# Performance work log

Hardware: AMD Instinct MI355X
Metric: run time of the kernel (lower is better)

## Reference

```python
import jax, jax.numpy as jnp
import numpy as np

N = 4_194_304
DT = 1800.0   # dt_s (30-minute steps)
G = 0.76      # solar transmittance g
AZ = 41.3     # glazed area Az


def setup_inputs() -> dict:
    key = jax.random.key(0)
    ks = jax.random.split(key, 16)
    f32 = jnp.float32
    def pos(k, lo, hi):  # positive scalar param
        return jax.random.uniform(k, (), dtype=f32, minval=lo, maxval=hi)
    return {
        # RC parameters (physically positive)
        "R_ie": pos(ks[0], 0.5, 2.0),
        "R_ea": pos(ks[1], 0.5, 2.0),
        "C_in": pos(ks[2], 1e6, 5e6),
        "C_en": pos(ks[3], 1e7, 5e7),
        "a_sol_in": pos(ks[4], 0.1, 0.9),
        "a_sol_en": pos(ks[5], 0.1, 0.9),
        "a_int_in": pos(ks[6], 0.1, 0.9),
        "a_int_en": pos(ks[7], 0.1, 0.9),
        "Tin0": jax.random.uniform(ks[8], (), dtype=f32, minval=18.0, maxval=22.0),
        # driver time series
        "To": jax.random.normal(ks[9], (N,), dtype=f32) * 5.0 + 10.0,
        "Irr": jax.random.uniform(ks[10], (N,), dtype=f32, maxval=800.0),
        "Qint": jax.random.uniform(ks[11], (N,), dtype=f32, maxval=500.0),
        "Qah": jax.random.uniform(ks[12], (N,), dtype=f32, maxval=3000.0),
        "Ria": jax.random.uniform(ks[13], (N,), dtype=f32, minval=0.05, maxval=0.5),
    }


def _simulate(R_ie, R_ea, C_in, C_en, a_sol_in, a_sol_en, a_int_in, a_int_en,
              Tin0, To, Irr, Qint, Qah, Ria):
    dt = jnp.float32(DT)
    Ria_c = jnp.maximum(Ria, 1e-6)                      # (n,)
    # A matrix entries (A22 varies per step via Ria)
    A11 = -(1.0 / R_ea + 1.0 / R_ie) / C_en             # scalar
    A12 = (1.0 / R_ie) / C_en                           # scalar
    A21 = (1.0 / R_ie) / C_in                           # scalar
    A22 = -(1.0 / Ria_c + 1.0 / R_ie) / C_in            # (n,)
    # M = I - dt*A, closed-form 2x2 inverse via determinant
    M11 = 1.0 - dt * A11                                # scalar
    M12 = -dt * A12                                     # scalar
    M21 = -dt * A21                                     # scalar
    M22 = 1.0 - dt * A22                                # (n,)
    det = M11 * M22 - M12 * M21                         # (n,)
    # dt * B @ u, vectorized over all steps
    Qsol = (G * AZ) * Irr                               # (n,)
    bu0 = dt * (To / (C_en * R_ea) + (a_sol_en / C_en) * Qsol + (a_int_en / C_en) * Qint)
    bu1 = dt * (To / (C_in * Ria_c) + (a_sol_in / C_in) * Qsol + (a_int_in / C_in) * Qint + Qah / C_in)

    def step(x, inp):
        b0, b1, m22, d = inp
        r0 = x[0] + b0
        r1 = x[1] + b1
        xn0 = (m22 * r0 - M12 * r1) / d
        xn1 = (-M21 * r0 + M11 * r1) / d
        return jnp.stack([xn0, xn1]), xn1

    x0 = jnp.stack([Tin0, Tin0])
    _, Tin_seq = jax.lax.scan(step, x0, (bu0, bu1, M22, det))
    return Tin_seq                                      # (n,) indoor temps


def reference(R_ie, R_ea, C_in, C_en, a_sol_in, a_sol_en, a_int_in, a_int_en,
              Tin0, To, Irr, Qint, Qah, Ria):
    return _simulate(R_ie, R_ea, C_in, C_en, a_sol_in, a_sol_en, a_int_in, a_int_en,
                     Tin0, To, Irr, Qint, Qah, Ria)
```

## Files before the change

kernel.cpp:

```cpp
#include <hip/hip_runtime.h>

#define BLOCK 256
#define SPAN_LB 4096
#define KITER 4
#define SPAN_FB 4096

struct Xf { float p, q, r, s, u, v; };

__device__ __forceinline__ Xf xf_id() {
    Xf t; t.p = 1.f; t.q = 0.f; t.r = 0.f; t.s = 1.f; t.u = 0.f; t.v = 0.f;
    return t;
}

__device__ __forceinline__ Xf xf_compose(const Xf& E, const Xf& L) {
    Xf o;
    o.p = L.p * E.p + L.q * E.r;
    o.q = L.p * E.q + L.q * E.s;
    o.r = L.r * E.p + L.s * E.r;
    o.s = L.r * E.q + L.s * E.s;
    o.u = L.p * E.u + L.q * E.v + L.u;
    o.v = L.r * E.u + L.s * E.v + L.v;
    return o;
}

struct Par {
    float M11, M12, M21, Kx;
    float c0, c1;
    float cTo0, cIrr0, cQi0;
    float cIrr1, cQi1;
};

__device__ __forceinline__ Par make_par(
    const float* pRie, const float* pRea, const float* pCin, const float* pCen,
    const float* pAsi, const float* pAse, const float* pAii, const float* pAie)
{
    const float dt = 1800.0f;
    const float GA = 0.76f * 41.3f;
    float R_ie = *pRie, R_ea = *pRea, C_in = *pCin, C_en = *pCen;
    float asi = *pAsi, ase = *pAse, aii = *pAii, aie = *pAie;
    Par P;
    float iRie = 1.0f / R_ie;
    P.M11 = 1.0f + dt * (1.0f / R_ea + iRie) / C_en;
    P.M12 = -(dt * iRie) / C_en;
    P.M21 = -(dt * iRie) / C_in;
    P.Kx  = P.M12 * P.M21;
    P.c1  = dt / C_in;
    P.c0  = 1.0f + P.c1 * iRie;
    P.cTo0  = dt / (C_en * R_ea);
    P.cIrr0 = dt * ase * GA / C_en;
    P.cQi0  = dt * aie / C_en;
    P.cIrr1 = dt * asi * GA / C_in;
    P.cQi1  = dt * aii / C_in;
    return P;
}

__device__ __forceinline__ void storeA(float* A, int s, const Xf& v) {
    float* b = A + 6 * s + (s >> 2);
    b[0] = v.p; b[1] = v.q; b[2] = v.r; b[3] = v.s; b[4] = v.u; b[5] = v.v;
}
__device__ __forceinline__ Xf loadA(const float* A, int s) {
    const float* b = A + 6 * s + (s >> 2);
    Xf v; v.p = b[0]; v.q = b[1]; v.r = b[2]; v.s = b[3]; v.u = b[4]; v.v = b[5];
    return v;
}
__device__ __forceinline__ void sm_store(float* sm, int i, const Xf& v) {
    float* b = sm + i * 7;
    b[0] = v.p; b[1] = v.q; b[2] = v.r; b[3] = v.s; b[4] = v.u; b[5] = v.v;
}
__device__ __forceinline__ Xf sm_load(const float* sm, int i) {
    const float* b = sm + i * 7;
    Xf v; v.p = b[0]; v.q = b[1]; v.r = b[2]; v.s = b[3]; v.u = b[4]; v.v = b[5];
    return v;
}

__device__ __forceinline__ Xf block_scan(Xf v, float* sm) {
    const int t = threadIdx.x;
    sm_store(sm, t, v);
    __syncthreads();
    for (int off = 1; off < BLOCK; off <<= 1) {
        Xf e;
        bool has = (t >= off);
        if (has) e = sm_load(sm, t - off);
        __syncthreads();
        if (has) { v = xf_compose(e, v); sm_store(sm, t, v); }
        __syncthreads();
    }
    return v;
}

__global__ __launch_bounds__(BLOCK, 4) void k_scan(
    const float* __restrict__ To, const float* __restrict__ Irr,
    const float* __restrict__ Qi, const float* __restrict__ Qa,
    const float* __restrict__ Ra,
    const float* pRie, const float* pRea, const float* pCin, const float* pCen,
    const float* pAsi, const float* pAse, const float* pAii, const float* pAie,
    const float* pTin0,
    unsigned int* __restrict__ flags, float* __restrict__ aggs,
    float* __restrict__ out, int N)
{
    __shared__ float smA[6400];
    __shared__ float smScan[BLOCK * 7];
    __shared__ float smE[6];
    const int t = threadIdx.x;
    const int b = blockIdx.x;
    const int blockBase = b * SPAN_LB;
    Par P = make_par(pRie, pRea, pCin, pCen, pAsi, pAse, pAii, pAie);

    float rRv[KITER][4], b0v[KITER][4], b1v[KITER][4];

#pragma unroll
    for (int k = 0; k < KITER; ++k) {
        const int s = t + BLOCK * k;
        const int gstep = blockBase + s * 4;
        float tox[4], irx[4], qix[4], qax[4], rax[4];
        if (gstep + 4 <= N) {
            float4 v;
            v = *(const float4*)(To  + gstep); tox[0]=v.x; tox[1]=v.y; tox[2]=v.z; tox[3]=v.w;
            v = *(const float4*)(Irr + gstep); irx[0]=v.x; irx[1]=v.y; irx[2]=v.z; irx[3]=v.w;
            v = *(const float4*)(Qi  + gstep); qix[0]=v.x; qix[1]=v.y; qix[2]=v.z; qix[3]=v.w;
            v = *(const float4*)(Qa  + gstep); qax[0]=v.x; qax[1]=v.y; qax[2]=v.z; qax[3]=v.w;
            v = *(const float4*)(Ra  + gstep); rax[0]=v.x; rax[1]=v.y; rax[2]=v.z; rax[3]=v.w;
        } else {
#pragma unroll
            for (int j = 0; j < 4; ++j) {
                int gi = gstep + j; bool val = gi < N;
                tox[j] = val ? To[gi]  : 0.f;
                irx[j] = val ? Irr[gi] : 0.f;
                qix[j] = val ? Qi[gi]  : 0.f;
                qax[j] = val ? Qa[gi]  : 0.f;
                rax[j] = val ? Ra[gi]  : 1.f;
            }
        }
        Xf sub = xf_id();
#pragma unroll
        for (int j = 0; j < 4; ++j) {
            float rR = __builtin_amdgcn_rcpf(fmaxf(rax[j], 1e-6f));
            float b0 = P.cTo0 * tox[j] + P.cIrr0 * irx[j] + P.cQi0 * qix[j];
            float b1 = P.c1 * fmaf(tox[j], rR, qax[j]) + P.cIrr1 * irx[j] + P.cQi1 * qix[j];
            rRv[k][j] = rR; b0v[k][j] = b0; b1v[k][j] = b1;
            if (gstep + j < N) {
                float M22 = fmaf(P.c1, rR, P.c0);
                float det = fmaf(P.M11, M22, -P.Kx);
                float rd  = __builtin_amdgcn_rcpf(det);
                Xf T;
                T.p =  M22 * rd;
                T.q = -P.M12 * rd;
                T.r = -P.M21 * rd;
                T.s =  P.M11 * rd;
                T.u = T.p * b0 + T.q * b1;
                T.v = T.r * b0 + T.s * b1;
                sub = xf_compose(sub, T);
            }
        }
        storeA(smA, s, sub);
    }
    __syncthreads();

    Xf w = xf_id();
#pragma unroll
    for (int j = 0; j < KITER; ++j) w = xf_compose(w, loadA(smA, KITER * t + j));
    Xf incl = block_scan(w, smScan);
    Xf E = (t > 0) ? sm_load(smScan, t - 1) : xf_id();

    if (t == BLOCK - 1) {
        float* dst = aggs + 6 * b;
        __hip_atomic_store(dst + 0, incl.p, __ATOMIC_RELAXED, __HIP_MEMORY_SCOPE_AGENT);
        __hip_atomic_store(dst + 1, incl.q, __ATOMIC_RELAXED, __HIP_MEMORY_SCOPE_AGENT);
        __hip_atomic_store(dst + 2, incl.r, __ATOMIC_RELAXED, __HIP_MEMORY_SCOPE_AGENT);
        __hip_atomic_store(dst + 3, incl.s, __ATOMIC_RELAXED, __HIP_MEMORY_SCOPE_AGENT);
        __hip_atomic_store(dst + 4, incl.u, __ATOMIC_RELAXED, __HIP_MEMORY_SCOPE_AGENT);
        __hip_atomic_store(dst + 5, incl.v, __ATOMIC_RELAXED, __HIP_MEMORY_SCOPE_AGENT);
        __hip_atomic_store(&flags[b], 1u, __ATOMIC_RELEASE, __HIP_MEMORY_SCOPE_AGENT);
    }

    if (b == 0) {
        if (t == 0) {
            smE[0] = 1.f; smE[1] = 0.f; smE[2] = 0.f;
            smE[3] = 1.f; smE[4] = 0.f; smE[5] = 0.f;
        }
    } else if (t < 64) {
        Xf acc = xf_id();
        for (int base = 0; base < b; base += 64) {
            const int idx = base + t;
            const bool has = (idx < b);
            for (;;) {
                bool ready = !has ||
                    (__hip_atomic_load(&flags[idx], __ATOMIC_ACQUIRE, __HIP_MEMORY_SCOPE_AGENT) != 0u);
                if (__all(ready)) break;
                __builtin_amdgcn_s_sleep(1);
            }
            Xf v = xf_id();
            if (has) {
                const float* src = aggs + 6 * idx;
                v.p = __hip_atomic_load(src + 0, __ATOMIC_RELAXED, __HIP_MEMORY_SCOPE_AGENT);
                v.q = __hip_atomic_load(src + 1, __ATOMIC_RELAXED, __HIP_MEMORY_SCOPE_AGENT);
                v.r = __hip_atomic_load(src + 2, __ATOMIC_RELAXED, __HIP_MEMORY_SCOPE_AGENT);
                v.s = __hip_atomic_load(src + 3, __ATOMIC_RELAXED, __HIP_MEMORY_SCOPE_AGENT);
                v.u = __hip_atomic_load(src + 4, __ATOMIC_RELAXED, __HIP_MEMORY_SCOPE_AGENT);
                v.v = __hip_atomic_load(src + 5, __ATOMIC_RELAXED, __HIP_MEMORY_SCOPE_AGENT);
            }
#pragma unroll
            for (int sft = 1; sft < 64; sft <<= 1) {
                Xf u;
                u.p = __shfl_up(v.p, sft, 64);
                u.q = __shfl_up(v.q, sft, 64);
                u.r = __shfl_up(v.r, sft, 64);
                u.s = __shfl_up(v.s, sft, 64);
                u.u = __shfl_up(v.u, sft, 64);
                u.v = __shfl_up(v.v, sft, 64);
                if (t >= sft) v = xf_compose(u, v);
            }
            Xf wacc;
            wacc.p = __shfl(v.p, 63, 64);
            wacc.q = __shfl(v.q, 63, 64);
            wacc.r = __shfl(v.r, 63, 64);
            wacc.s = __shfl(v.s, 63, 64);
            wacc.u = __shfl(v.u, 63, 64);
            wacc.v = __shfl(v.v, 63, 64);
            acc = xf_compose(acc, wacc);
        }
        if (t == 0) {
            smE[0] = acc.p; smE[1] = acc.q; smE[2] = acc.r;
            smE[3] = acc.s; smE[4] = acc.u; smE[5] = acc.v;
        }
    }
    __syncthreads();

    float T0 = *pTin0;
    float xb0 = (smE[0] + smE[1]) * T0 + smE[4];
    float xb1 = (smE[2] + smE[3]) * T0 + smE[5];

    float sx0 = E.p * xb0 + E.q * xb1 + E.u;
    float sx1 = E.r * xb0 + E.s * xb1 + E.v;
    float st0[KITER], st1[KITER];
#pragma unroll
    for (int j = 0; j < KITER; ++j) {
        st0[j] = sx0; st1[j] = sx1;
        Xf S = loadA(smA, KITER * t + j);
        float n0 = S.p * sx0 + S.q * sx1 + S.u;
        float n1 = S.r * sx0 + S.s * sx1 + S.v;
        sx0 = n0; sx1 = n1;
    }
    __syncthreads();
#pragma unroll
    for (int j = 0; j < KITER; ++j) {
        int s = KITER * t + j;
        float* pS = smA + 2 * s + (s >> 3);
        pS[0] = st0[j]; pS[1] = st1[j];
    }
    __syncthreads();

#pragma unroll
    for (int k = 0; k < KITER; ++k) {
        const int s = t + BLOCK * k;
        const float* pS = smA + 2 * s + (s >> 3);
        float x0 = pS[0], x1 = pS[1];
        const int gstep = blockBase + s * 4;
        float ov[4];
#pragma unroll
        for (int j = 0; j < 4; ++j) {
            float rR  = rRv[k][j];
            float M22 = fmaf(P.c1, rR, P.c0);
            float det = fmaf(P.M11, M22, -P.Kx);
            float rd  = __builtin_amdgcn_rcpf(det);
            float r0 = x0 + b0v[k][j];
            float r1 = x1 + b1v[k][j];
            float n0 = (M22 * r0 - P.M12 * r1) * rd;
            float n1 = (P.M11 * r1 - P.M21 * r0) * rd;
            x0 = n0; x1 = n1; ov[j] = n1;
        }
        if (gstep + 4 <= N) {
            float4 o; o.x = ov[0]; o.y = ov[1]; o.z = ov[2]; o.w = ov[3];
            *(float4*)(out + gstep) = o;
        } else {
#pragma unroll
            for (int j = 0; j < 4; ++j) { int gi = gstep + j; if (gi < N) out[gi] = ov[j]; }
        }
    }
}

__global__ __launch_bounds__(BLOCK, 4) void k_blocksum(
    const float* __restrict__ To, const float* __restrict__ Irr,
    const float* __restrict__ Qi, const float* __restrict__ Qa,
    const float* __restrict__ Ra,
    const float* pRie, const float* pRea, const float* pCin, const float* pCen,
    const float* pAsi, const float* pAse, const float* pAii, const float* pAie,
    Xf* __restrict__ blkX, int N)
{
    __shared__ float smA[6400];
    __shared__ float smScan[BLOCK * 7];
    const int t = threadIdx.x;
    const int blockBase = blockIdx.x * SPAN_FB;
    Par P = make_par(pRie, pRea, pCin, pCen, pAsi, pAse, pAii, pAie);

#pragma unroll
    for (int k = 0; k < 4; ++k) {
        const int s = t + BLOCK * k;
        const int gstep = blockBase + s * 4;
        float tox[4], irx[4], qix[4], qax[4], rax[4];
        if (gstep + 4 <= N) {
            float4 v;
            v = *(const float4*)(To  + gstep); tox[0]=v.x; tox[1]=v.y; tox[2]=v.z; tox[3]=v.w;
            v = *(const float4*)(Irr + gstep); irx[0]=v.x; irx[1]=v.y; irx[2]=v.z; irx[3]=v.w;
            v = *(const float4*)(Qi  + gstep); qix[0]=v.x; qix[1]=v.y; qix[2]=v.z; qix[3]=v.w;
            v = *(const float4*)(Qa  + gstep); qax[0]=v.x; qax[1]=v.y; qax[2]=v.z; qax[3]=v.w;
            v = *(const float4*)(Ra  + gstep); rax[0]=v.x; rax[1]=v.y; rax[2]=v.z; rax[3]=v.w;
        } else {
#pragma unroll
            for (int j = 0; j < 4; ++j) {
                int gi = gstep + j; bool val = gi < N;
                tox[j] = val ? To[gi]  : 0.f;
                irx[j] = val ? Irr[gi] : 0.f;
                qix[j] = val ? Qi[gi]  : 0.f;
                qax[j] = val ? Qa[gi]  : 0.f;
                rax[j] = val ? Ra[gi]  : 1.f;
            }
        }
        Xf sub = xf_id();
#pragma unroll
        for (int j = 0; j < 4; ++j) {
            if (gstep + j < N) {
                float rR  = __builtin_amdgcn_rcpf(fmaxf(rax[j], 1e-6f));
                float b0  = P.cTo0 * tox[j] + P.cIrr0 * irx[j] + P.cQi0 * qix[j];
                float b1  = P.c1 * fmaf(tox[j], rR, qax[j]) + P.cIrr1 * irx[j] + P.cQi1 * qix[j];
                float M22 = fmaf(P.c1, rR, P.c0);
                float det = fmaf(P.M11, M22, -P.Kx);
                float rd  = __builtin_amdgcn_rcpf(det);
                Xf T;
                T.p =  M22 * rd;
                T.q = -P.M12 * rd;
                T.r = -P.M21 * rd;
                T.s =  P.M11 * rd;
                T.u = T.p * b0 + T.q * b1;
                T.v = T.r * b0 + T.s * b1;
                sub = xf_compose(sub, T);
            }
        }
        storeA(smA, s, sub);
    }
    __syncthreads();

    Xf w = xf_id();
#pragma unroll
    for (int j = 0; j < 4; ++j) w = xf_compose(w, loadA(smA, 4 * t + j));
    Xf incl = block_scan(w, smScan);
    if (t == BLOCK - 1) blkX[blockIdx.x] = incl;
}

__global__ __launch_bounds__(BLOCK) void k_mid(
    const Xf* __restrict__ blkX, float2* __restrict__ blkSt,
    const float* pTin0, int NB)
{
    const int t = threadIdx.x;
    const int ser = (NB + BLOCK - 1) / BLOCK;
    const int base = t * ser;
    Xf acc = xf_id();
    for (int j = 0; j < ser; ++j) {
        int i = base + j;
        if (i < NB) acc = xf_compose(acc, blkX[i]);
    }
    __shared__ float sm[BLOCK * 7];
    block_scan(acc, sm);
    Xf E = xf_id();
    if (t > 0) E = sm_load(sm, t - 1);
    float T0 = *pTin0;
    float x0 = (E.p + E.q) * T0 + E.u;
    float x1 = (E.r + E.s) * T0 + E.v;
    for (int j = 0; j < ser; ++j) {
        int i = base + j;
        if (i < NB) {
            blkSt[i] = make_float2(x0, x1);
            Xf T = blkX[i];
            float n0 = T.p * x0 + T.q * x1 + T.u;
            float n1 = T.r * x0 + T.s * x1 + T.v;
            x0 = n0; x1 = n1;
        }
    }
}

__global__ __launch_bounds__(BLOCK, 4) void k_emit(
    const float* __restrict__ To, const float* __restrict__ Irr,
    const float* __restrict__ Qi, const float* __restrict__ Qa,
    const float* __restrict__ Ra,
    const float* pRie, const float* pRea, const float* pCin, const float* pCen,
    const float* pAsi, const float* pAse, const float* pAii, const float* pAie,
    const float2* __restrict__ blkSt, float* __restrict__ out, int N)
{
    __shared__ float smA[6400];
    __shared__ float smScan[BLOCK * 7];
    const int t = threadIdx.x;
    const int b = blockIdx.x;
    const int blockBase = b * SPAN_FB;
    Par P = make_par(pRie, pRea, pCin, pCen, pAsi, pAse, pAii, pAie);

    float rRv[4][4], b0v[4][4], b1v[4][4];

#pragma unroll
    for (int k = 0; k < 4; ++k) {
        const int s = t + BLOCK * k;
        const int gstep = blockBase + s * 4;
        float tox[4], irx[4], qix[4], qax[4], rax[4];
        if (gstep + 4 <= N) {
            float4 v;
            v = *(const float4*)(To  + gstep); tox[0]=v.x; tox[1]=v.y; tox[2]=v.z; tox[3]=v.w;
            v = *(const float4*)(Irr + gstep); irx[0]=v.x; irx[1]=v.y; irx[2]=v.z; irx[3]=v.w;
            v = *(const float4*)(Qi  + gstep); qix[0]=v.x; qix[1]=v.y; qix[2]=v.z; qix[3]=v.w;
            v = *(const float4*)(Qa  + gstep); qax[0]=v.x; qax[1]=v.y; qax[2]=v.z; qax[3]=v.w;
            v = *(const float4*)(Ra  + gstep); rax[0]=v.x; rax[1]=v.y; rax[2]=v.z; rax[3]=v.w;
        } else {
#pragma unroll
            for (int j = 0; j < 4; ++j) {
                int gi = gstep + j; bool val = gi < N;
                tox[j] = val ? To[gi]  : 0.f;
                irx[j] = val ? Irr[gi] : 0.f;
                qix[j] = val ? Qi[gi]  : 0.f;
                qax[j] = val ? Qa[gi]  : 0.f;
                rax[j] = val ? Ra[gi]  : 1.f;
            }
        }
        Xf sub = xf_id();
#pragma unroll
        for (int j = 0; j < 4; ++j) {
            float rR = __builtin_amdgcn_rcpf(fmaxf(rax[j], 1e-6f));
            float b0 = P.cTo0 * tox[j] + P.cIrr0 * irx[j] + P.cQi0 * qix[j];
            float b1 = P.c1 * fmaf(tox[j], rR, qax[j]) + P.cIrr1 * irx[j] + P.cQi1 * qix[j];
            rRv[k][j] = rR; b0v[k][j] = b0; b1v[k][j] = b1;
            if (gstep + j < N) {
                float M22 = fmaf(P.c1, rR, P.c0);
                float det = fmaf(P.M11, M22, -P.Kx);
                float rd  = __builtin_amdgcn_rcpf(det);
                Xf T;
                T.p =  M22 * rd;
                T.q = -P.M12 * rd;
                T.r = -P.M21 * rd;
                T.s =  P.M11 * rd;
                T.u = T.p * b0 + T.q * b1;
                T.v = T.r * b0 + T.s * b1;
                sub = xf_compose(sub, T);
            }
        }
        storeA(smA, s, sub);
    }
    __syncthreads();

    Xf w = xf_id();
#pragma unroll
    for (int j = 0; j < 4; ++j) w = xf_compose(w, loadA(smA, 4 * t + j));
    block_scan(w, smScan);
    Xf E = (t > 0) ? sm_load(smScan, t - 1) : xf_id();

    float2 B = blkSt[b];
    float sx0 = E.p * B.x + E.q * B.y + E.u;
    float sx1 = E.r * B.x + E.s * B.y + E.v;
    float st0[4], st1[4];
#pragma unroll
    for (int j = 0; j < 4; ++j) {
        st0[j] = sx0; st1[j] = sx1;
        Xf S = loadA(smA, 4 * t + j);
        float n0 = S.p * sx0 + S.q * sx1 + S.u;
        float n1 = S.r * sx0 + S.s * sx1 + S.v;
        sx0 = n0; sx1 = n1;
    }
    __syncthreads();
#pragma unroll
    for (int j = 0; j < 4; ++j) {
        int s = 4 * t + j;
        float* pS = smA + 2 * s + (s >> 3);
        pS[0] = st0[j]; pS[1] = st1[j];
    }
    __syncthreads();

#pragma unroll
    for (int k = 0; k < 4; ++k) {
        const int s = t + BLOCK * k;
        const float* pS = smA + 2 * s + (s >> 3);
        float x0 = pS[0], x1 = pS[1];
        const int gstep = blockBase + s * 4;
        float ov[4];
#pragma unroll
        for (int j = 0; j < 4; ++j) {
            float rR  = rRv[k][j];
            float M22 = fmaf(P.c1, rR, P.c0);
            float det = fmaf(P.M11, M22, -P.Kx);
            float rd  = __builtin_amdgcn_rcpf(det);
            float r0 = x0 + b0v[k][j];
            float r1 = x1 + b1v[k][j];
            float n0 = (M22 * r0 - P.M12 * r1) * rd;
            float n1 = (P.M11 * r1 - P.M21 * r0) * rd;
            x0 = n0; x1 = n1; ov[j] = n1;
        }
        if (gstep + 4 <= N) {
            float4 o; o.x = ov[0]; o.y = ov[1]; o.z = ov[2]; o.w = ov[3];
            *(float4*)(out + gstep) = o;
        } else {
#pragma unroll
            for (int j = 0; j < 4; ++j) { int gi = gstep + j; if (gi < N) out[gi] = ov[j]; }
        }
    }
}

extern "C" void kernel_launch(void* const* d_in, const int* in_sizes, int n_in,
                              void* d_out, int out_size, void* d_ws, size_t ws_size,
                              hipStream_t stream)
{
    (void)n_in; (void)out_size; (void)ws_size;
    const float* pRie = (const float*)d_in[0];
    const float* pRea = (const float*)d_in[1];
    const float* pCin = (const float*)d_in[2];
    const float* pCen = (const float*)d_in[3];
    const float* pAsi = (const float*)d_in[4];
    const float* pAse = (const float*)d_in[5];
    const float* pAii = (const float*)d_in[6];
    const float* pAie = (const float*)d_in[7];
    const float* pTin0 = (const float*)d_in[8];
    const float* To  = (const float*)d_in[9];
    const float* Irr = (const float*)d_in[10];
    const float* Qi  = (const float*)d_in[11];
    const float* Qa  = (const float*)d_in[12];
    const float* Ra  = (const float*)d_in[13];
    float* outp = (float*)d_out;
    int N = in_sizes[9];
    if (N <= 0) return;

    const int NB = (N + SPAN_LB - 1) / SPAN_LB;

    int dev = 0;
    hipGetDevice(&dev);
    int numCU = 0;
    hipDeviceGetAttribute(&numCU, hipDeviceAttributeMultiprocessorCount, dev);
    int maxb = 0;
    hipOccupancyMaxActiveBlocksPerMultiprocessor(&maxb, (const void*)k_scan, BLOCK, 0);
    bool ok = (maxb > 0) && ((long long)maxb * (long long)numCU >= (long long)NB);

    if (ok) {
        unsigned int* flags = (unsigned int*)d_ws;
        size_t off = (((size_t)NB * 4) + 255) & ~(size_t)255;
        float* aggs = (float*)((char*)d_ws + off);
        hipMemsetAsync(flags, 0, (size_t)NB * 4, stream);
        k_scan<<<NB, BLOCK, 0, stream>>>(To, Irr, Qi, Qa, Ra,
            pRie, pRea, pCin, pCen, pAsi, pAse, pAii, pAie, pTin0,
            flags, aggs, outp, N);
    } else {
        const int NB3 = (N + SPAN_FB - 1) / SPAN_FB;
        Xf* blkX = (Xf*)d_ws;
        size_t off = ((size_t)NB3 * sizeof(Xf) + 255) & ~(size_t)255;
        float2* blkSt = (float2*)((char*)d_ws + off);
        k_blocksum<<<NB3, BLOCK, 0, stream>>>(To, Irr, Qi, Qa, Ra,
            pRie, pRea, pCin, pCen, pAsi, pAse, pAii, pAie, blkX, N);
        k_mid<<<1, BLOCK, 0, stream>>>(blkX, blkSt, pTin0, NB3);
        k_emit<<<NB3, BLOCK, 0, stream>>>(To, Irr, Qi, Qa, Ra,
            pRie, pRea, pCin, pCen, pAsi, pAse, pAii, pAie, blkSt, outp, N);
    }
}
```

Measured before the change: 47.58 us.

## Let block 0 compute all block start states and publish them

Previously each block scanned all predecessor aggregates itself with one wavefront, which costs O(b) work and waiting per block. Now block 0 waits for every block's aggregate, does a block-wide scan over them, and writes each block's starting state to global memory behind a second flag array. Other blocks only spin on their own flag and read two floats. This makes block 0 a serial bottleneck that must wait for the last block's aggregate before anyone can finish. It also limits the fast path to NB <= 1024.

```diff
diff --git a/kernel.cpp b/kernel.cpp
--- a/kernel.cpp
+++ b/kernel.cpp
@@ -88,6 +88,18 @@
     return v;
 }
 
+__device__ __forceinline__ Xf agg_load(const float* aggs, int idx) {
+    const float* src = aggs + 6 * idx;
+    Xf v;
+    v.p = __hip_atomic_load(src + 0, __ATOMIC_RELAXED, __HIP_MEMORY_SCOPE_AGENT);
+    v.q = __hip_atomic_load(src + 1, __ATOMIC_RELAXED, __HIP_MEMORY_SCOPE_AGENT);
+    v.r = __hip_atomic_load(src + 2, __ATOMIC_RELAXED, __HIP_MEMORY_SCOPE_AGENT);
+    v.s = __hip_atomic_load(src + 3, __ATOMIC_RELAXED, __HIP_MEMORY_SCOPE_AGENT);
+    v.u = __hip_atomic_load(src + 4, __ATOMIC_RELAXED, __HIP_MEMORY_SCOPE_AGENT);
+    v.v = __hip_atomic_load(src + 5, __ATOMIC_RELAXED, __HIP_MEMORY_SCOPE_AGENT);
+    return v;
+}
+
 __global__ __launch_bounds__(BLOCK, 4) void k_scan(
     const float* __restrict__ To, const float* __restrict__ Irr,
     const float* __restrict__ Qi, const float* __restrict__ Qa,
@@ -95,12 +107,15 @@
     const float* pRie, const float* pRea, const float* pCin, const float* pCen,
     const float* pAsi, const float* pAse, const float* pAii, const float* pAie,
     const float* pTin0,
-    unsigned int* __restrict__ flags, float* __restrict__ aggs,
-    float* __restrict__ out, int N)
+    unsigned int* __restrict__ flags1,
+    unsigned int* __restrict__ flags2,
+    float* __restrict__ aggs,
+    float* __restrict__ states,
+    float* __restrict__ out, int N, int NB)
 {
     __shared__ float smA[6400];
     __shared__ float smScan[BLOCK * 7];
-    __shared__ float smE[6];
+    __shared__ float smE[2];
     const int t = threadIdx.x;
     const int b = blockIdx.x;
     const int blockBase = b * SPAN_LB;
@@ -170,65 +185,55 @@
         __hip_atomic_store(dst + 3, incl.s, __ATOMIC_RELAXED, __HIP_MEMORY_SCOPE_AGENT);
         __hip_atomic_store(dst + 4, incl.u, __ATOMIC_RELAXED, __HIP_MEMORY_SCOPE_AGENT);
         __hip_atomic_store(dst + 5, incl.v, __ATOMIC_RELAXED, __HIP_MEMORY_SCOPE_AGENT);
-        __hip_atomic_store(&flags[b], 1u, __ATOMIC_RELEASE, __HIP_MEMORY_SCOPE_AGENT);
+        __hip_atomic_store(&flags1[b], 1u, __ATOMIC_RELEASE, __HIP_MEMORY_SCOPE_AGENT);
     }
 
     if (b == 0) {
-        if (t == 0) {
-            smE[0] = 1.f; smE[1] = 0.f; smE[2] = 0.f;
-            smE[3] = 1.f; smE[4] = 0.f; smE[5] = 0.f;
-        }
-    } else if (t < 64) {
-        Xf acc = xf_id();
-        for (int base = 0; base < b; base += 64) {
-            const int idx = base + t;
-            const bool has = (idx < b);
-            for (;;) {
-                bool ready = !has ||
-                    (__hip_atomic_load(&flags[idx], __ATOMIC_ACQUIRE, __HIP_MEMORY_SCOPE_AGENT) != 0u);
-                if (__all(ready)) break;
-                __builtin_amdgcn_s_sleep(1);
-            }
-            Xf v = xf_id();
-            if (has) {
-                const float* src = aggs + 6 * idx;
-                v.p = __hip_atomic_load(src + 0, __ATOMIC_RELAXED, __HIP_MEMORY_SCOPE_AGENT);
-                v.q = __hip_atomic_load(src + 1, __ATOMIC_RELAXED, __HIP_MEMORY_SCOPE_AGENT);
-                v.r = __hip_atomic_load(src + 2, __ATOMIC_RELAXED, __HIP_MEMORY_SCOPE_AGENT);
-                v.s = __hip_atomic_load(src + 3, __ATOMIC_RELAXED, __HIP_MEMORY_SCOPE_AGENT);
-                v.u = __hip_atomic_load(src + 4, __ATOMIC_RELAXED, __HIP_MEMORY_SCOPE_AGENT);
-                v.v = __hip_atomic_load(src + 5, __ATOMIC_RELAXED, __HIP_MEMORY_SCOPE_AGENT);
-            }
-#pragma unroll
-            for (int sft = 1; sft < 64; sft <<= 1) {
-                Xf u;
-                u.p = __shfl_up(v.p, sft, 64);
-                u.q = __shfl_up(v.q, sft, 64);
-                u.r = __shfl_up(v.r, sft, 64);
-                u.s = __shfl_up(v.s, sft, 64);
-                u.u = __shfl_up(v.u, sft, 64);
-                u.v = __shfl_up(v.v, sft, 64);
-                if (t >= sft) v = xf_compose(u, v);
-            }
-            Xf wacc;
-            wacc.p = __shfl(v.p, 63, 64);
-            wacc.q = __shfl(v.q, 63, 64);
-            wacc.r = __shfl(v.r, 63, 64);
-            wacc.s = __shfl(v.s, 63, 64);
-            wacc.u = __shfl(v.u, 63, 64);
-            wacc.v = __shfl(v.v, 63, 64);
-            acc = xf_compose(acc, wacc);
-        }
-        if (t == 0) {
-            smE[0] = acc.p; smE[1] = acc.q; smE[2] = acc.r;
-            smE[3] = acc.s; smE[4] = acc.u; smE[5] = acc.v;
-        }
-    }
-    __syncthreads();
-
-    float T0 = *pTin0;
-    float xb0 = (smE[0] + smE[1]) * T0 + smE[4];
-    float xb1 = (smE[2] + smE[3]) * T0 + smE[5];
+        const int i0 = 4 * t;
+#pragma unroll
+        for (int j = 0; j < 4; ++j) {
+            int idx = i0 + j;
+            if (idx < NB) {
+                while (__hip_atomic_load(&flags1[idx], __ATOMIC_ACQUIRE,
+                                         __HIP_MEMORY_SCOPE_AGENT) == 0u)
+                    __builtin_amdgcn_s_sleep(1);
+            }
+        }
+        Xf th = xf_id();
+#pragma unroll
+        for (int j = 0; j < 4; ++j) {
+            int idx = i0 + j;
+            if (idx < NB) th = xf_compose(th, agg_load(aggs, idx));
+        }
+        block_scan(th, smScan);
+        Xf Eb = (t > 0) ? sm_load(smScan, t - 1) : xf_id();
+        float T0 = *pTin0;
+        float s0 = (Eb.p + Eb.q) * T0 + Eb.u;
+        float s1 = (Eb.r + Eb.s) * T0 + Eb.v;
+        for (int j = 0; j < 4; ++j) {
+            int idx = i0 + j;
+            if (idx < NB) {
+                __hip_atomic_store(&states[2 * idx + 0], s0, __ATOMIC_RELAXED, __HIP_MEMORY_SCOPE_AGENT);
+                __hip_atomic_store(&states[2 * idx + 1], s1, __ATOMIC_RELAXED, __HIP_MEMORY_SCOPE_AGENT);
+                __hip_atomic_store(&flags2[idx], 1u, __ATOMIC_RELEASE, __HIP_MEMORY_SCOPE_AGENT);
+                Xf g = agg_load(aggs, idx);
+                float n0 = g.p * s0 + g.q * s1 + g.u;
+                float n1 = g.r * s0 + g.s * s1 + g.v;
+                s0 = n0; s1 = n1;
+            }
+        }
+    }
+
+    if (t == 0) {
+        while (__hip_atomic_load(&flags2[b], __ATOMIC_ACQUIRE,
+                                 __HIP_MEMORY_SCOPE_AGENT) == 0u)
+            __builtin_amdgcn_s_sleep(2);
+        smE[0] = __hip_atomic_load(&states[2 * b + 0], __ATOMIC_RELAXED, __HIP_MEMORY_SCOPE_AGENT);
+        smE[1] = __hip_atomic_load(&states[2 * b + 1], __ATOMIC_RELAXED, __HIP_MEMORY_SCOPE_AGENT);
+    }
+    __syncthreads();
+    float xb0 = smE[0];
+    float xb1 = smE[1];
 
     float sx0 = E.p * xb0 + E.q * xb1 + E.u;
     float sx1 = E.r * xb0 + E.s * xb1 + E.v;
@@ -530,16 +535,20 @@
     hipDeviceGetAttribute(&numCU, hipDeviceAttributeMultiprocessorCount, dev);
     int maxb = 0;
     hipOccupancyMaxActiveBlocksPerMultiprocessor(&maxb, (const void*)k_scan, BLOCK, 0);
-    bool ok = (maxb > 0) && ((long long)maxb * (long long)numCU >= (long long)NB);
+    bool ok = (maxb > 0) && ((long long)maxb * (long long)numCU >= (long long)NB)
+              && (NB <= 4 * BLOCK);
 
     if (ok) {
-        unsigned int* flags = (unsigned int*)d_ws;
-        size_t off = (((size_t)NB * 4) + 255) & ~(size_t)255;
-        float* aggs = (float*)((char*)d_ws + off);
-        hipMemsetAsync(flags, 0, (size_t)NB * 4, stream);
+        unsigned int* flags1 = (unsigned int*)d_ws;
+        unsigned int* flags2 = flags1 + NB;
+        size_t offA = (((size_t)NB * 8) + 255) & ~(size_t)255;
+        float* aggs = (float*)((char*)d_ws + offA);
+        size_t offS = offA + ((((size_t)NB * 24) + 255) & ~(size_t)255);
+        float* states = (float*)((char*)d_ws + offS);
+        hipMemsetAsync(flags1, 0, (size_t)NB * 8, stream);
         k_scan<<<NB, BLOCK, 0, stream>>>(To, Irr, Qi, Qa, Ra,
             pRie, pRea, pCin, pCen, pAsi, pAse, pAii, pAie, pTin0,
-            flags, aggs, outp, N);
+            flags1, flags2, aggs, states, outp, N, NB);
     } else {
         const int NB3 = (N + SPAN_FB - 1) / SPAN_FB;
         Xf* blkX = (Xf*)d_ws;
```

Result: no change. 47.34 us (-0.5%).
